# Kernel optimization log

Hardware: AMD Instinct MI355X
Metric: run time of the kernel (lower is better)

The kernel has to match this reference:

```python
import jax, jax.numpy as jnp
import numpy as np

D_MODEL = 1024; EXPAND = 2; D_INNER = 2048; D_STATE = 64; NGROUPS = 1
HEADDIM = 64; NHEADS = 32; D_CONV = 7; CHUNK = 256
CONV_DIM = D_INNER + 2 * NGROUPS * D_STATE            # 2176
D_IN_PROJ = 2 * D_INNER + 2 * NGROUPS * D_STATE + NHEADS  # 4256


def setup_inputs() -> dict:
    key = jax.random.key(0)
    ks = jax.random.split(key, 8)
    B, L = 2, 4096
    u = jax.random.normal(ks[0], (B, L, D_MODEL), jnp.float32)
    in_proj_w = jax.random.normal(ks[1], (D_IN_PROJ, D_MODEL), jnp.float32) * (1.0 / np.sqrt(D_MODEL))
    kscale = 1.0 / np.sqrt(D_CONV)
    conv_w = jax.random.uniform(ks[2], (CONV_DIM, 1, D_CONV), jnp.float32, -kscale, kscale)
    conv_b = jax.random.uniform(ks[3], (CONV_DIM,), jnp.float32, -kscale, kscale)
    # dt_bias init exactly as in the torch module
    dt = jnp.exp(jax.random.uniform(ks[4], (NHEADS,), jnp.float32) * (np.log(0.1) - np.log(0.001)) + np.log(0.001))
    dt = jnp.clip(dt, 1e-4)
    dt_bias = dt + jnp.log(-jnp.expm1(-dt))
    A_log = jnp.zeros((NHEADS,), jnp.float32)  # A = 1 -> A_log = 0, as in torch init
    norm_w = jnp.ones((D_INNER,), jnp.float32)
    out_proj_w = jax.random.normal(ks[5], (D_MODEL, D_INNER), jnp.float32) * (1.0 / np.sqrt(D_INNER))
    return {"u": u, "in_proj_w": in_proj_w, "conv_w": conv_w, "conv_b": conv_b,
            "dt_bias": dt_bias, "A_log": A_log, "norm_w": norm_w, "out_proj_w": out_proj_w}


def _segsum(x):
    # x: (..., T) -> (..., T, T) lower-triangular cumulative segment sums
    T = x.shape[-1]
    cs = jnp.cumsum(x, axis=-1)
    ss = cs[..., :, None] - cs[..., None, :]
    mask = jnp.tril(jnp.ones((T, T), bool))
    return jnp.where(mask, ss, -jnp.inf)


def _ssd(X, A, Bm, Cm, chunk):
    # Causal chunked SSD scan (Mamba2 'ssd_minimal_discrete').
    # X: (b,l,h,p) already multiplied by dt; A: (b,l,h) = A_h*dt; Bm/Cm: (b,l,h,n)
    b, l, h, p = X.shape
    n = Bm.shape[-1]
    c = l // chunk
    Xc = X.reshape(b, c, chunk, h, p)
    Ac = jnp.transpose(A.reshape(b, c, chunk, h), (0, 3, 1, 2))  # (b,h,c,l)
    Bc = Bm.reshape(b, c, chunk, h, n)
    Cc = Cm.reshape(b, c, chunk, h, n)
    A_cum = jnp.cumsum(Ac, axis=-1)
    Ldec = jnp.exp(_segsum(Ac))                                   # (b,h,c,l,s)
    G = jnp.einsum('bclhn,bcshn->bhcls', Cc, Bc)
    Y_diag = jnp.einsum('bhcls,bcshp->bclhp', G * Ldec, Xc)
    decay_states = jnp.exp(A_cum[..., -1:] - A_cum)               # (b,h,c,l)
    states = jnp.einsum('bclhn,bhcl,bclhp->bchpn', Bc, decay_states, Xc)
    A_last = jnp.pad(A_cum[..., -1], ((0, 0), (0, 0), (1, 0)))    # (b,h,c+1)
    decay_chunk = jnp.exp(_segsum(A_last))                        # (b,h,c+1,c+1)
    states = jnp.concatenate([jnp.zeros_like(states[:, :1]), states], axis=1)
    prev = jnp.einsum('bhzc,bchpn->bzhpn', decay_chunk, states)[:, :-1]
    Y_off = jnp.einsum('bclhn,bchpn,bhcl->bclhp', Cc, prev, jnp.exp(A_cum))
    return (Y_diag + Y_off).reshape(b, l, h, p)


def reference(u, in_proj_w, conv_w, conv_b, dt_bias, A_log, norm_w, out_proj_w):
    b, l, _ = u.shape
    zxbcdt = u @ in_proj_w.T                                      # (b,l,4256)
    z = zxbcdt[..., :D_INNER]
    xBC = zxbcdt[..., D_INNER:D_INNER + CONV_DIM]
    dt = jax.nn.softplus(zxbcdt[..., D_INNER + CONV_DIM:] + dt_bias)  # (b,l,h)
    # depthwise causal-padded conv1d ('same' padding, kernel 7)
    xBC = jax.lax.conv_general_dilated(
        jnp.transpose(xBC, (0, 2, 1)), conv_w, (1,), [(D_CONV // 2, D_CONV // 2)],
        dimension_numbers=('NCH', 'OIH', 'NCH'), feature_group_count=CONV_DIM)
    xBC = jax.nn.silu(jnp.transpose(xBC + conv_b[None, :, None], (0, 2, 1)))
    x = xBC[..., :D_INNER].reshape(b, l, NHEADS, HEADDIM)
    Bm = xBC[..., D_INNER:D_INNER + NGROUPS * D_STATE].reshape(b, l, NGROUPS, D_STATE)
    Cm = xBC[..., D_INNER + NGROUPS * D_STATE:].reshape(b, l, NGROUPS, D_STATE)
    Bm = jnp.repeat(Bm, NHEADS // NGROUPS, axis=2)                # broadcast groups to heads
    Cm = jnp.repeat(Cm, NHEADS // NGROUPS, axis=2)
    A = -jnp.exp(A_log)                                           # (h,)
    a = dt * A                                                    # (b,l,h)
    Xdt = x * dt[..., None]
    y_f = _ssd(Xdt, a, Bm, Cm, CHUNK)
    flip = lambda t: t[:, ::-1]
    y_b = flip(_ssd(flip(Xdt), flip(a), flip(Bm), flip(Cm), CHUNK))
    # bidirectional combine: fwd + bwd minus double-counted t==s diagonal term
    diag = jnp.einsum('blhn,blhn->blh', Cm, Bm)[..., None] * Xdt
    y = (y_f + y_b - diag).reshape(b, l, D_INNER)
    # RMSNormGated with norm_before_gate=True: rmsnorm(y) * w * silu(z)
    rstd = jax.lax.rsqrt(jnp.mean(y * y, axis=-1, keepdims=True) + 1e-5)
    y = (y * rstd) * norm_w * jax.nn.silu(z)
    return y @ out_proj_w.T
```

## Files before the change

### kernel.cpp

```cpp
#include <hip/hip_runtime.h>
#include <math.h>

#define BB 2
#define LL 4096
#define DM 1024
#define DI 2048
#define NH 32
#define HD 64
#define NSTATE 64
#define CONVD 2176
#define RAWC 2208
#define NC 16
#define CK 256
#define CTL 128

typedef __attribute__((ext_vector_type(8))) short bf16x8;
typedef __attribute__((ext_vector_type(8))) _Float16 f16x8;
typedef __attribute__((ext_vector_type(4))) float f32x4;

#define WAITVM(N) asm volatile("s_waitcnt vmcnt(" #N ")" ::: "memory")
#define WAITLGKM0 asm volatile("s_waitcnt lgkmcnt(0)" ::: "memory")

__device__ __forceinline__ float sigmoidf_(float x) { return 1.f / (1.f + expf(-x)); }
__device__ __forceinline__ float softplusf_(float x) { return (x > 20.f) ? x : log1pf(expf(x)); }

__device__ __forceinline__ unsigned short f2bf(float v) {
    unsigned u = __float_as_uint(v);
    unsigned r = (u + 0x7FFFu + ((u >> 16) & 1u)) >> 16;
    return (unsigned short)r;
}
__device__ __forceinline__ float bf2f(unsigned short h) {
    return __uint_as_float(((unsigned)h) << 16);
}

__device__ __forceinline__ int swz(int row, int col) {
    return row * 64 + ((((col >> 3) ^ (row & 7)) << 3) | (col & 7));
}

typedef const __attribute__((address_space(1))) void gvoid_t;
typedef __attribute__((address_space(3))) void lvoid_t;
__device__ __forceinline__ void gload_lds16(const void* g, void* l) {
    __builtin_amdgcn_global_load_lds((gvoid_t*)g, (lvoid_t*)l, 16, 0, 0);
}


__global__ __launch_bounds__(256) void pack_a16(const float* __restrict__ X,
                                                _Float16* __restrict__ Y, int n) {
    int idx = blockIdx.x * 256 + threadIdx.x;
    if (idx < n) Y[idx] = (_Float16)X[idx];
}

__global__ __launch_bounds__(256) void pack_w16(const float* __restrict__ W,
                                                _Float16* __restrict__ Y,
                                                int N, int Npad, int K) {
    int idx = blockIdx.x * 256 + threadIdx.x;
    if (idx >= Npad * K) return;
    int n = idx / K;
    Y[idx] = (n < N) ? (_Float16)W[idx] : (_Float16)0.f;
}

__global__ __launch_bounds__(256) void gemm_f16(const _Float16* __restrict__ A,
                                                const _Float16* __restrict__ B,
                                                float* __restrict__ C,
                                                int M, int N, int K) {
    __shared__ _Float16 As[128 * 32];
    __shared__ _Float16 Bs[128 * 32];
    int tid = threadIdx.x;
    int lane = tid & 63;
    int w = tid >> 6;
    int wr = w >> 1, wc = w & 1;
    int n0 = blockIdx.x * 128, m0 = blockIdx.y * 128;
    f32x4 acc[4][4] = {};

    for (int k0 = 0; k0 < K; k0 += 32) {
        #pragma unroll
        for (int p = 0; p < 2; ++p) {
            int s = p * 256 + tid;
            int row = s >> 2;
            int sub = (s & 3) ^ ((row >> 1) & 3);
            gload_lds16(A + (size_t)(m0 + row) * K + k0 + sub * 8, &As[s * 8]);
            gload_lds16(B + (size_t)(n0 + row) * K + k0 + sub * 8, &Bs[s * 8]);
        }
        __syncthreads();
        f16x8 af[4], bfv[4];
        #pragma unroll
        for (int i = 0; i < 4; ++i) {
            int rowA = wr * 64 + i * 16 + (lane & 15);
            int slotA = (lane >> 4) ^ ((rowA >> 1) & 3);
            af[i] = *(const f16x8*)&As[rowA * 32 + slotA * 8];
            int rowB = wc * 64 + i * 16 + (lane & 15);
            int slotB = (lane >> 4) ^ ((rowB >> 1) & 3);
            bfv[i] = *(const f16x8*)&Bs[rowB * 32 + slotB * 8];
        }
        #pragma unroll
        for (int i = 0; i < 4; ++i)
            #pragma unroll
            for (int j = 0; j < 4; ++j)
                acc[i][j] = __builtin_amdgcn_mfma_f32_16x16x32_f16(af[i], bfv[j], acc[i][j], 0, 0, 0);
        __syncthreads();
    }

    #pragma unroll
    for (int i = 0; i < 4; ++i) {
        int mbase = m0 + wr * 64 + i * 16 + (lane >> 4) * 4;
        #pragma unroll
        for (int j = 0; j < 4; ++j) {
            int n = n0 + wc * 64 + j * 16 + (lane & 15);
            if (n < N) {
                #pragma unroll
                for (int r = 0; r < 4; ++r)
                    C[(size_t)(mbase + r) * N + n] = acc[i][j][r];
            }
        }
    }
}


__global__ __launch_bounds__(256) void conv_silu(const float* __restrict__ raw,
                                                 const float* __restrict__ cw,
                                                 const float* __restrict__ cb,
                                                 float* __restrict__ xbc) {
    int ch = blockIdx.x * 256 + threadIdx.x;
    if (ch >= CONVD) return;
    int l0 = blockIdx.y * CTL;
    int b = blockIdx.z;
    float wt[7];
    #pragma unroll
    for (int j = 0; j < 7; ++j) wt[j] = cw[ch * 7 + j];
    float bias = cb[ch];
    const float* rbase = raw + (size_t)b * LL * RAWC + ch;
    float win[7];
    #pragma unroll
    for (int j = 0; j < 6; ++j) {
        int lj = l0 - 3 + j;
        win[j] = (lj >= 0 && lj < LL) ? rbase[(size_t)lj * RAWC] : 0.f;
    }
    size_t obase = ((size_t)b * LL + l0) * CONVD + ch;
    for (int i = 0; i < CTL; ++i) {
        int lj = l0 + i + 3;
        win[6] = (lj < LL) ? rbase[(size_t)lj * RAWC] : 0.f;
        float acc = bias;
        #pragma unroll
        for (int j = 0; j < 7; ++j) acc += wt[j] * win[j];
        xbc[obase + (size_t)i * CONVD] = acc * sigmoidf_(acc);
        #pragma unroll
        for (int j = 0; j < 6; ++j) win[j] = win[j + 1];
    }
}

__global__ __launch_bounds__(256) void dt_kernel(const float* __restrict__ raw,
                                                 const float* __restrict__ dt_bias,
                                                 float* __restrict__ dtb) {
    int idx = blockIdx.x * 256 + threadIdx.x;
    if (idx >= BB * LL * NH) return;
    int h = idx & 31;
    int row = idx >> 5;
    float x = raw[(size_t)row * RAWC + CONVD + h] + dt_bias[h];
    dtb[idx] = softplusf_(x);
}


__device__ __forceinline__ float block_scan256(float v, float* sc, int tid) {
    sc[tid] = v;
    __syncthreads();
    for (int off = 1; off < 256; off <<= 1) {
        float t = 0.f;
        if (tid >= off) t = sc[tid - off];
        __syncthreads();
        sc[tid] += t;
        __syncthreads();
    }
    return sc[tid];
}

__global__ __launch_bounds__(256) void g_mfma(const float* __restrict__ xbc,
                                              unsigned short* __restrict__ Gth,
                                              unsigned short* __restrict__ Gtl,
                                              int dir) {
    int lt = blockIdx.x, st = blockIdx.y, bc = blockIdx.z;
    if (st > lt) return;
    int b = bc / NC, c = bc % NC;
    int tid = threadIdx.x, lane = tid & 63, w = tid >> 6;
    __shared__ short Ch[4096], Cl[4096], Bh[4096], Bl[4096];
    #pragma unroll
    for (int i = 0; i < 16; ++i) {
        int e = tid + i * 256;
        int r = e >> 6, q = e & 63;
        int il = c * CK + lt * 64 + r;
        int tl = dir ? (LL - 1 - il) : il;
        float cv = xbc[((size_t)b * LL + tl) * CONVD + DI + NSTATE + q];
        unsigned short chh = f2bf(cv);
        Ch[swz(r, q)] = chh;
        Cl[swz(r, q)] = f2bf(cv - bf2f(chh));
        int is = c * CK + st * 64 + r;
        int ts = dir ? (LL - 1 - is) : is;
        float bv = xbc[((size_t)b * LL + ts) * CONVD + DI + q];
        unsigned short bhh = f2bf(bv);
        Bh[swz(r, q)] = bhh;
        Bl[swz(r, q)] = f2bf(bv - bf2f(bhh));
    }
    __syncthreads();
    f32x4 acc[4] = {};
    #pragma unroll
    for (int kk = 0; kk < 64; kk += 32) {
        int arow = w * 16 + (lane & 15);
        int aslot = ((kk >> 3) + (lane >> 4)) ^ (arow & 7);
        bf16x8 ah = *(const bf16x8*)&Ch[arow * 64 + aslot * 8];
        bf16x8 al = *(const bf16x8*)&Cl[arow * 64 + aslot * 8];
        #pragma unroll
        for (int j = 0; j < 4; ++j) {
            int brow = j * 16 + (lane & 15);
            int bslot = ((kk >> 3) + (lane >> 4)) ^ (brow & 7);
            bf16x8 bh = *(const bf16x8*)&Bh[brow * 64 + bslot * 8];
            bf16x8 bl = *(const bf16x8*)&Bl[brow * 64 + bslot * 8];
            acc[j] = __builtin_amdgcn_mfma_f32_16x16x32_bf16(ah, bh, acc[j], 0, 0, 0);
            acc[j] = __builtin_amdgcn_mfma_f32_16x16x32_bf16(ah, bl, acc[j], 0, 0, 0);
            acc[j] = __builtin_amdgcn_mfma_f32_16x16x32_bf16(al, bh, acc[j], 0, 0, 0);
        }
    }
    size_t tbase = ((size_t)bc * 10 + (size_t)(lt * (lt + 1) / 2 + st)) * 4096;
    #pragma unroll
    for (int j = 0; j < 4; ++j)
        #pragma unroll
        for (int rr = 0; rr < 4; ++rr) {
            int row = w * 16 + (lane >> 4) * 4 + rr;
            int col = j * 16 + (lane & 15);
            float g = acc[j][rr];
            if (lt == st && (col + dir > row)) g = 0.f;
            unsigned short hi = f2bf(g);
            int si = swz(row, col);
            Gth[tbase + si] = hi;
            Gtl[tbase + si] = f2bf(g - bf2f(hi));
        }
}

__global__ __launch_bounds__(256) void s1_mfma(const float* __restrict__ xbc,
                                               const float* __restrict__ dtb,
                                               const float* __restrict__ A_log,
                                               float* __restrict__ states,
                                               float* __restrict__ csum, int dir) {
    int h = blockIdx.x, c = blockIdx.y, b = blockIdx.z;
    int tid = threadIdx.x, lane = tid & 63, w = tid >> 6;
    __shared__ float sc[256];
    {
        int gi = c * CK + tid;
        int t = dir ? (LL - 1 - gi) : gi;
        float A = -expf(A_log[h]);
        float dtv = dtb[((size_t)b * LL + t) * NH + h];
        float acum = block_scan256(dtv * A, sc, tid);
        float cs = sc[255];
        if (tid == 0) csum[(b * NC + c) * NH + h] = cs;
        float wgt = expf(cs - acum) * dtv;
        __syncthreads();
        sc[tid] = wgt;
        __syncthreads();
    }
    __shared__ short XTh[4096], XTl[4096], BTh[4096], BTl[4096];
    f32x4 acc[4] = {};
    #pragma unroll
    for (int st = 0; st < 4; ++st) {
        #pragma unroll
        for (int i = 0; i < 16; ++i) {
            int e = tid + i * 256;
            int r = e >> 6, q = e & 63;
            int gs = c * CK + st * 64 + r;
            int ts = dir ? (LL - 1 - gs) : gs;
            size_t rowb = ((size_t)b * LL + ts) * CONVD;
            float xv = xbc[rowb + h * 64 + q] * sc[st * 64 + r];
            unsigned short xh = f2bf(xv);
            XTh[swz(q, r)] = xh;
            XTl[swz(q, r)] = f2bf(xv - bf2f(xh));
            float bv = xbc[rowb + DI + q];
            unsigned short bh_ = f2bf(bv);
            BTh[swz(q, r)] = bh_;
            BTl[swz(q, r)] = f2bf(bv - bf2f(bh_));
        }
        __syncthreads();
        #pragma unroll
        for (int kk = 0; kk < 64; kk += 32) {
            int arow = w * 16 + (lane & 15);
            int aslot = ((kk >> 3) + (lane >> 4)) ^ (arow & 7);
            bf16x8 ah = *(const bf16x8*)&XTh[arow * 64 + aslot * 8];
            bf16x8 al = *(const bf16x8*)&XTl[arow * 64 + aslot * 8];
            #pragma unroll
            for (int j = 0; j < 4; ++j) {
                int brow = j * 16 + (lane & 15);
                int bslot = ((kk >> 3) + (lane >> 4)) ^ (brow & 7);
                bf16x8 bh = *(const bf16x8*)&BTh[brow * 64 + bslot * 8];
                bf16x8 bl = *(const bf16x8*)&BTl[brow * 64 + bslot * 8];
                acc[j] = __builtin_amdgcn_mfma_f32_16x16x32_bf16(ah, bh, acc[j], 0, 0, 0);
                acc[j] = __builtin_amdgcn_mfma_f32_16x16x32_bf16(ah, bl, acc[j], 0, 0, 0);
                acc[j] = __builtin_amdgcn_mfma_f32_16x16x32_bf16(al, bh, acc[j], 0, 0, 0);
            }
        }
        __syncthreads();
    }
    size_t base = (((size_t)(b * NC + c) * NH + h)) * 4096;
    #pragma unroll
    for (int j = 0; j < 4; ++j)
        #pragma unroll
        for (int rr = 0; rr < 4; ++rr) {
            int p = w * 16 + (lane >> 4) * 4 + rr;
            int n = j * 16 + (lane & 15);
            states[base + p * 64 + n] = acc[j][rr];
        }
}

__global__ __launch_bounds__(256) void s2_scan(float* __restrict__ states,
                                               const float* __restrict__ csum) {
    int h = blockIdx.x, b = blockIdx.y, eo = blockIdx.z;
    int e = eo * 256 + threadIdx.x;
    float run = 0.f;
    for (int z = 0; z < NC; ++z) {
        size_t base = (((size_t)(b * NC + z) * NH + h)) * (64 * 64);
        float s = states[base + e];
        states[base + e] = run;
        float g = expf(csum[(b * NC + z) * NH + h]);
        run = run * g + s;
    }
}

__global__ __launch_bounds__(256) void s3_pipe(const float* __restrict__ xbc,
                                               const float* __restrict__ dtb,
                                               const float* __restrict__ A_log,
                                               const unsigned short* __restrict__ Gth,
                                               const unsigned short* __restrict__ Gtl,
                                               const float* __restrict__ prev,
                                               float* __restrict__ y, int dir, int beta) {
    int h = blockIdx.x, bc = blockIdx.y;
    int b = bc / NC, c = bc % NC;
    int tid = threadIdx.x, lane = tid & 63, w = tid >> 6;

    __shared__ short Xh[4][4096], Xl[4][4096];
    __shared__ short Gh[3][4096], Gl[3][4096];
    __shared__ float sEl[256], sEin[256];

    {
        int gi = c * CK + tid;
        int t = dir ? (LL - 1 - gi) : gi;
        float A = -expf(A_log[h]);
        float dtv = dtb[((size_t)b * LL + t) * NH + h];
        float acum = block_scan256(dtv * A, sEl, tid);
        sEl[tid] = expf(acum);
        sEin[tid] = expf(-acum) * dtv;
    }
    __syncthreads();

    constexpr int tri_[10] = {0, 1, 3, 6, 2, 4, 7, 5, 8, 9};
    auto issueA = [&](int i) {
        size_t tb = ((size_t)bc * 10 + tri_[i]) * 4096;
        int slot = i % 3;
        int o = w * 1024 + lane * 8;
        gload_lds16(Gth + tb + o,       &Gh[slot][o]);
        gload_lds16(Gth + tb + o + 512, &Gh[slot][o + 512]);
        gload_lds16(Gtl + tb + o,       &Gl[slot][o]);
        gload_lds16(Gtl + tb + o + 512, &Gl[slot][o + 512]);
    };
    issueA(0); issueA(1); issueA(2);

    #pragma unroll
    for (int st = 0; st < 4; ++st)
        #pragma unroll
        for (int i2 = 0; i2 < 16; ++i2) {
            int e = tid + i2 * 256;
            int r = e >> 6, q = e & 63;
            int gs = c * CK + st * 64 + r;
            int ts = dir ? (LL - 1 - gs) : gs;
            float xv = xbc[((size_t)b * LL + ts) * CONVD + h * 64 + q] * sEin[st * 64 + r];
            unsigned short xh = f2bf(xv);
            Xh[st][swz(q, r)] = xh;
            Xl[st][swz(q, r)] = f2bf(xv - bf2f(xh));
        }

    __builtin_amdgcn_sched_barrier(0);
    WAITLGKM0;
    __builtin_amdgcn_s_barrier();

    f32x4 acc[4][4] = {};
    constexpr int ph_lq[10] = {0, 1, 2, 3, 1, 2, 3, 2, 3, 3};
    constexpr int ph_st[10] = {0, 0, 0, 0, 1, 1, 1, 2, 2, 3};
    #pragma unroll
    for (int i = 0; i < 10; ++i) {
        const int lq = ph_lq[i], st = ph_st[i], slot = i % 3;
        if (i < 8)       { WAITVM(8); }
        else if (i == 8) { WAITVM(4); }
        else             { WAITVM(0); }
        __builtin_amdgcn_sched_barrier(0);
        int arow = w * 16 + (lane & 15);
        int s0 = (lane >> 4) ^ (arow & 7);
        int s1 = (4 + (lane >> 4)) ^ (arow & 7);
        bf16x8 ah0 = *(const bf16x8*)&Gh[slot][arow * 64 + s0 * 8];
        bf16x8 al0 = *(const bf16x8*)&Gl[slot][arow * 64 + s0 * 8];
        bf16x8 ah1 = *(const bf16x8*)&Gh[slot][arow * 64 + s1 * 8];
        bf16x8 al1 = *(const bf16x8*)&Gl[slot][arow * 64 + s1 * 8];
        bf16x8 bh0[4], bl0[4], bh1[4], bl1[4];
        #pragma unroll
        for (int j = 0; j < 4; ++j) {
            int brow = j * 16 + (lane & 15);
            int t0 = (lane >> 4) ^ (brow & 7);
            int t1 = (4 + (lane >> 4)) ^ (brow & 7);
            bh0[j] = *(const bf16x8*)&Xh[st][brow * 64 + t0 * 8];
            bl0[j] = *(const bf16x8*)&Xl[st][brow * 64 + t0 * 8];
            bh1[j] = *(const bf16x8*)&Xh[st][brow * 64 + t1 * 8];
            bl1[j] = *(const bf16x8*)&Xl[st][brow * 64 + t1 * 8];
        }
        WAITLGKM0;
        __builtin_amdgcn_sched_barrier(0);
        if (i + 3 < 10) issueA(i + 3);
        __builtin_amdgcn_sched_barrier(0);
        #pragma unroll
        for (int j = 0; j < 4; ++j) {
            acc[lq][j] = __builtin_amdgcn_mfma_f32_16x16x32_bf16(ah0, bh0[j], acc[lq][j], 0, 0, 0);
            acc[lq][j] = __builtin_amdgcn_mfma_f32_16x16x32_bf16(ah0, bl0[j], acc[lq][j], 0, 0, 0);
            acc[lq][j] = __builtin_amdgcn_mfma_f32_16x16x32_bf16(al0, bh0[j], acc[lq][j], 0, 0, 0);
            acc[lq][j] = __builtin_amdgcn_mfma_f32_16x16x32_bf16(ah1, bh1[j], acc[lq][j], 0, 0, 0);
            acc[lq][j] = __builtin_amdgcn_mfma_f32_16x16x32_bf16(ah1, bl1[j], acc[lq][j], 0, 0, 0);
            acc[lq][j] = __builtin_amdgcn_mfma_f32_16x16x32_bf16(al1, bh1[j], acc[lq][j], 0, 0, 0);
        }
    }

    __syncthreads();
    {
        size_t pbase = ((size_t)bc * NH + h) * 4096;
        #pragma unroll
        for (int i2 = 0; i2 < 16; ++i2) {
            int e = tid + i2 * 256;
            int r = e >> 6, q = e & 63;
            float pv = prev[pbase + r * 64 + q];
            unsigned short ph = f2bf(pv);
            Xh[0][swz(r, q)] = ph;
            Xl[0][swz(r, q)] = f2bf(pv - bf2f(ph));
            int il = c * CK + r;
            int tl = dir ? (LL - 1 - il) : il;
            float cv = xbc[((size_t)b * LL + tl) * CONVD + DI + NSTATE + q];
            unsigned short chh = f2bf(cv);
            Gh[0][swz(r, q)] = chh;
            Gl[0][swz(r, q)] = f2bf(cv - bf2f(chh));
        }
        __syncthreads();
        #pragma unroll
        for (int lq = 0; lq < 4; ++lq) {
            if (lq < 3) {
                #pragma unroll
                for (int i2 = 0; i2 < 16; ++i2) {
                    int e = tid + i2 * 256;
                    int r = e >> 6, q = e & 63;
                    int il = c * CK + (lq + 1) * 64 + r;
                    int tl = dir ? (LL - 1 - il) : il;
                    float cv = xbc[((size_t)b * LL + tl) * CONVD + DI + NSTATE + q];
                    unsigned short chh = f2bf(cv);
                    Gh[(lq + 1) & 1][swz(r, q)] = chh;
                    Gl[(lq + 1) & 1][swz(r, q)] = f2bf(cv - bf2f(chh));
                }
            }
            int arow = w * 16 + (lane & 15);
            int s0 = (lane >> 4) ^ (arow & 7);
            int s1 = (4 + (lane >> 4)) ^ (arow & 7);
            bf16x8 ah0 = *(const bf16x8*)&Gh[lq & 1][arow * 64 + s0 * 8];
            bf16x8 al0 = *(const bf16x8*)&Gl[lq & 1][arow * 64 + s0 * 8];
            bf16x8 ah1 = *(const bf16x8*)&Gh[lq & 1][arow * 64 + s1 * 8];
            bf16x8 al1 = *(const bf16x8*)&Gl[lq & 1][arow * 64 + s1 * 8];
            #pragma unroll
            for (int j = 0; j < 4; ++j) {
                int brow = j * 16 + (lane & 15);
                int t0 = (lane >> 4) ^ (brow & 7);
                int t1 = (4 + (lane >> 4)) ^ (brow & 7);
                bf16x8 bh0 = *(const bf16x8*)&Xh[0][brow * 64 + t0 * 8];
                bf16x8 bl0 = *(const bf16x8*)&Xl[0][brow * 64 + t0 * 8];
                bf16x8 bh1 = *(const bf16x8*)&Xh[0][brow * 64 + t1 * 8];
                bf16x8 bl1 = *(const bf16x8*)&Xl[0][brow * 64 + t1 * 8];
                acc[lq][j] = __builtin_amdgcn_mfma_f32_16x16x32_bf16(ah0, bh0, acc[lq][j], 0, 0, 0);
                acc[lq][j] = __builtin_amdgcn_mfma_f32_16x16x32_bf16(ah0, bl0, acc[lq][j], 0, 0, 0);
                acc[lq][j] = __builtin_amdgcn_mfma_f32_16x16x32_bf16(al0, bh0, acc[lq][j], 0, 0, 0);
                acc[lq][j] = __builtin_amdgcn_mfma_f32_16x16x32_bf16(ah1, bh1, acc[lq][j], 0, 0, 0);
                acc[lq][j] = __builtin_amdgcn_mfma_f32_16x16x32_bf16(ah1, bl1, acc[lq][j], 0, 0, 0);
                acc[lq][j] = __builtin_amdgcn_mfma_f32_16x16x32_bf16(al1, bh1, acc[lq][j], 0, 0, 0);
            }
            __syncthreads();
        }
    }

    #pragma unroll
    for (int lq = 0; lq < 4; ++lq)
        #pragma unroll
        for (int j = 0; j < 4; ++j)
            #pragma unroll
            for (int rr = 0; rr < 4; ++rr) {
                int ll = lq * 64 + w * 16 + (lane >> 4) * 4 + rr;
                int il = c * CK + ll;
                int tl = dir ? (LL - 1 - il) : il;
                size_t yb = ((size_t)b * LL + tl) * DI + h * 64 + j * 16 + (lane & 15);
                float v = sEl[ll] * acc[lq][j][rr];
                if (beta) y[yb] += v;
                else      y[yb]  = v;
            }
}

__global__ __launch_bounds__(256) void norm_gate16(const float* __restrict__ zbuf,
                                                   const float* __restrict__ norm_w,
                                                   const float* __restrict__ y,
                                                   _Float16* __restrict__ y16) {
    int row = blockIdx.x;
    int tid = threadIdx.x;
    float ss = 0.f;
    size_t yb = (size_t)row * DI;
    for (int i = tid; i < DI; i += 256) {
        float v = y[yb + i];
        ss += v * v;
    }
    #pragma unroll
    for (int off = 32; off > 0; off >>= 1) ss += __shfl_down(ss, off, 64);
    __shared__ float red[4];
    if ((tid & 63) == 0) red[tid >> 6] = ss;
    __syncthreads();
    float tot = red[0] + red[1] + red[2] + red[3];
    float rstd = rsqrtf(tot / DI + 1e-5f);
    for (int i = tid; i < DI; i += 256) {
        float z = zbuf[yb + i];
        float g = z * sigmoidf_(z);
        y16[yb + i] = (_Float16)(y[yb + i] * rstd * norm_w[i] * g);
    }
}

extern "C" void kernel_launch(void* const* d_in, const int* in_sizes, int n_in,
                              void* d_out, int out_size, void* d_ws, size_t ws_size,
                              hipStream_t stream) {
    const float* u          = (const float*)d_in[0];
    const float* in_proj_w  = (const float*)d_in[1];
    const float* conv_w     = (const float*)d_in[2];
    const float* conv_b     = (const float*)d_in[3];
    const float* dt_bias    = (const float*)d_in[4];
    const float* A_log      = (const float*)d_in[5];
    const float* norm_w     = (const float*)d_in[6];
    const float* out_proj_w = (const float*)d_in[7];
    float* out = (float*)d_out;

    float* ws  = (float*)d_ws;
    float* z   = ws;
    float* raw = z + (size_t)BB * LL * DI;
    float* xbc = raw + (size_t)BB * LL * RAWC;
    float* y   = raw;

    _Float16* u16    = (_Float16*)d_out;
    _Float16* w16z   = (_Float16*)xbc;
    _Float16* w16raw = w16z + (size_t)2048 * 1024;
    _Float16* w16out = (_Float16*)xbc;
    _Float16* y16    = w16out + (size_t)1024 * 2048;

    float* states        = (float*)d_out;
    unsigned short* Gth  = (unsigned short*)(states + 4194304);
    unsigned short* Gtl  = Gth + 2621440;
    float* dtb           = (float*)(Gtl + 2621440);
    float* csum          = dtb + 262144;
    float* prev          = states;

    dim3 blk(256);
    int M = BB * LL;

    pack_a16<<<(M * DM + 255) / 256, blk, 0, stream>>>(u, u16, M * DM);
    pack_w16<<<(2048 * DM + 255) / 256, blk, 0, stream>>>(in_proj_w, w16z, 2048, 2048, DM);
    pack_w16<<<(2304 * DM + 255) / 256, blk, 0, stream>>>(in_proj_w + (size_t)DI * DM, w16raw, RAWC, 2304, DM);
    gemm_f16<<<dim3(2048 / 128, M / 128), blk, 0, stream>>>(u16, w16z, z, M, 2048, DM);
    gemm_f16<<<dim3(2304 / 128, M / 128), blk, 0, stream>>>(u16, w16raw, raw, M, RAWC, DM);
    conv_silu<<<dim3((CONVD + 255) / 256, LL / CTL, BB), blk, 0, stream>>>(raw, conv_w, conv_b, xbc);
    dt_kernel<<<(BB * LL * NH + 255) / 256, blk, 0, stream>>>(raw, dt_bias, dtb);
    for (int dir = 0; dir < 2; ++dir) {
        g_mfma<<<dim3(4, 4, BB * NC), blk, 0, stream>>>(xbc, Gth, Gtl, dir);
        s1_mfma<<<dim3(NH, NC, BB), blk, 0, stream>>>(xbc, dtb, A_log, states, csum, dir);
        s2_scan<<<dim3(NH, BB, 16), blk, 0, stream>>>(states, csum);
        s3_pipe<<<dim3(NH, BB * NC), blk, 0, stream>>>(xbc, dtb, A_log, Gth, Gtl, prev, y, dir, dir);
    }
    norm_gate16<<<M, blk, 0, stream>>>(z, norm_w, y, y16);
    pack_a16<<<(DM * DI + 255) / 256, blk, 0, stream>>>(out_proj_w, w16out, DM * DI);
    gemm_f16<<<dim3(1024 / 128, M / 128), blk, 0, stream>>>(y16, w16out, out, M, DM, DI);
}
```

Measured before the change: 688.0 us.

## Double-buffer X and G tiles in s3_pipe to fit two blocks per CU

s3_pipe previously staged all four X sub-tiles (hi and lo bf16) plus a triple-buffered G pipeline in LDS, about 114 KB per block. That allowed only one block per CU. The change keeps two X slots and two G slots, refilling X sub-tiles inside the MFMA loop with extra barriers at phase boundaries, and sets launch_bounds(256,2). The goal is to fit two resident blocks per CU so one block's global-load latency can hide behind the other's MFMAs. The cost is a shallower prefetch, more block-wide barriers, and X conversion work serialized into the compute loop.

```diff
diff --git a/kernel.cpp b/kernel.cpp
--- a/kernel.cpp
+++ b/kernel.cpp
@@ -320,19 +320,19 @@
     }
 }
 
-__global__ __launch_bounds__(256) void s3_pipe(const float* __restrict__ xbc,
-                                               const float* __restrict__ dtb,
-                                               const float* __restrict__ A_log,
-                                               const unsigned short* __restrict__ Gth,
-                                               const unsigned short* __restrict__ Gtl,
-                                               const float* __restrict__ prev,
-                                               float* __restrict__ y, int dir, int beta) {
+__global__ __launch_bounds__(256, 2) void s3_pipe(const float* __restrict__ xbc,
+                                                  const float* __restrict__ dtb,
+                                                  const float* __restrict__ A_log,
+                                                  const unsigned short* __restrict__ Gth,
+                                                  const unsigned short* __restrict__ Gtl,
+                                                  const float* __restrict__ prev,
+                                                  float* __restrict__ y, int dir, int beta) {
     int h = blockIdx.x, bc = blockIdx.y;
     int b = bc / NC, c = bc % NC;
     int tid = threadIdx.x, lane = tid & 63, w = tid >> 6;
 
-    __shared__ short Xh[4][4096], Xl[4][4096];
-    __shared__ short Gh[3][4096], Gl[3][4096];
+    __shared__ short Xh[2][4096], Xl[2][4096];
+    __shared__ short Gh[2][4096], Gl[2][4096];
     __shared__ float sEl[256], sEin[256];
 
     {
@@ -349,17 +349,15 @@
     constexpr int tri_[10] = {0, 1, 3, 6, 2, 4, 7, 5, 8, 9};
     auto issueA = [&](int i) {
         size_t tb = ((size_t)bc * 10 + tri_[i]) * 4096;
-        int slot = i % 3;
+        int slot = i & 1;
         int o = w * 1024 + lane * 8;
         gload_lds16(Gth + tb + o,       &Gh[slot][o]);
         gload_lds16(Gth + tb + o + 512, &Gh[slot][o + 512]);
         gload_lds16(Gtl + tb + o,       &Gl[slot][o]);
         gload_lds16(Gtl + tb + o + 512, &Gl[slot][o + 512]);
     };
-    issueA(0); issueA(1); issueA(2);
-
-    #pragma unroll
-    for (int st = 0; st < 4; ++st)
+    auto stageX = [&](int st) {
+        int slot = st & 1;
         #pragma unroll
         for (int i2 = 0; i2 < 16; ++i2) {
             int e = tid + i2 * 256;
@@ -368,9 +366,13 @@
             int ts = dir ? (LL - 1 - gs) : gs;
             float xv = xbc[((size_t)b * LL + ts) * CONVD + h * 64 + q] * sEin[st * 64 + r];
             unsigned short xh = f2bf(xv);
-            Xh[st][swz(q, r)] = xh;
-            Xl[st][swz(q, r)] = f2bf(xv - bf2f(xh));
-        }
+            Xh[slot][swz(q, r)] = xh;
+            Xl[slot][swz(q, r)] = f2bf(xv - bf2f(xh));
+        }
+    };
+
+    issueA(0); issueA(1);
+    stageX(0);
 
     __builtin_amdgcn_sched_barrier(0);
     WAITLGKM0;
@@ -381,10 +383,14 @@
     constexpr int ph_st[10] = {0, 0, 0, 0, 1, 1, 1, 2, 2, 3};
     #pragma unroll
     for (int i = 0; i < 10; ++i) {
-        const int lq = ph_lq[i], st = ph_st[i], slot = i % 3;
-        if (i < 8)       { WAITVM(8); }
-        else if (i == 8) { WAITVM(4); }
-        else             { WAITVM(0); }
+        const int lq = ph_lq[i], st = ph_st[i], slot = i & 1, xslot = st & 1;
+        if (i == 4 || i == 7 || i == 9) {
+            __builtin_amdgcn_sched_barrier(0);
+            WAITLGKM0;
+            __builtin_amdgcn_s_barrier();
+        }
+        if (i < 9) { WAITVM(4); }
+        else       { WAITVM(0); }
         __builtin_amdgcn_sched_barrier(0);
         int arow = w * 16 + (lane & 15);
         int s0 = (lane >> 4) ^ (arow & 7);
@@ -399,15 +405,18 @@
             int brow = j * 16 + (lane & 15);
             int t0 = (lane >> 4) ^ (brow & 7);
             int t1 = (4 + (lane >> 4)) ^ (brow & 7);
-            bh0[j] = *(const bf16x8*)&Xh[st][brow * 64 + t0 * 8];
-            bl0[j] = *(const bf16x8*)&Xl[st][brow * 64 + t0 * 8];
-            bh1[j] = *(const bf16x8*)&Xh[st][brow * 64 + t1 * 8];
-            bl1[j] = *(const bf16x8*)&Xl[st][brow * 64 + t1 * 8];
+            bh0[j] = *(const bf16x8*)&Xh[xslot][brow * 64 + t0 * 8];
+            bl0[j] = *(const bf16x8*)&Xl[xslot][brow * 64 + t0 * 8];
+            bh1[j] = *(const bf16x8*)&Xh[xslot][brow * 64 + t1 * 8];
+            bl1[j] = *(const bf16x8*)&Xl[xslot][brow * 64 + t1 * 8];
         }
         WAITLGKM0;
         __builtin_amdgcn_sched_barrier(0);
-        if (i + 3 < 10) issueA(i + 3);
+        if (i + 2 < 10) issueA(i + 2);
         __builtin_amdgcn_sched_barrier(0);
+        if (i == 0)      stageX(1);
+        else if (i == 4) stageX(2);
+        else if (i == 7) stageX(3);
         #pragma unroll
         for (int j = 0; j < 4; ++j) {
             acc[lq][j] = __builtin_amdgcn_mfma_f32_16x16x32_bf16(ah0, bh0[j], acc[lq][j], 0, 0, 0);
```

Measured after the change: 764.7 us. 1.11x slower.

## Load G and C operands directly into registers instead of staging through LDS

Applied to the files above, without the earlier changes.

The s3 kernel stops staging the precomputed G tiles through a triple-buffered async global-to-LDS pipeline. Each wave now loads its MFMA A-operand fragments straight from global memory into registers, and g_mfma writes G unswizzled to match. The C-matrix operand for the inter-chunk term is likewise read from global and split into hi/lo bf16 in registers, replacing the LDS double-buffer and its per-iteration barriers. This cuts LDS use (raising occupancy) and removes syncs, but exposes global-load latency with no explicit prefetch and issues strided, uncoalesced float reads for C.

```diff
diff --git a/kernel.cpp b/kernel.cpp
--- a/kernel.cpp
+++ b/kernel.cpp
@@ -17,9 +17,6 @@
 typedef __attribute__((ext_vector_type(8))) short bf16x8;
 typedef __attribute__((ext_vector_type(8))) _Float16 f16x8;
 typedef __attribute__((ext_vector_type(4))) float f32x4;
-
-#define WAITVM(N) asm volatile("s_waitcnt vmcnt(" #N ")" ::: "memory")
-#define WAITLGKM0 asm volatile("s_waitcnt lgkmcnt(0)" ::: "memory")
 
 __device__ __forceinline__ float sigmoidf_(float x) { return 1.f / (1.f + expf(-x)); }
 __device__ __forceinline__ float softplusf_(float x) { return (x > 20.f) ? x : log1pf(expf(x)); }
@@ -228,7 +225,7 @@
             float g = acc[j][rr];
             if (lt == st && (col + dir > row)) g = 0.f;
             unsigned short hi = f2bf(g);
-            int si = swz(row, col);
+            int si = row * 64 + col;
             Gth[tbase + si] = hi;
             Gtl[tbase + si] = f2bf(g - bf2f(hi));
         }
@@ -320,19 +317,18 @@
     }
 }
 
-__global__ __launch_bounds__(256) void s3_pipe(const float* __restrict__ xbc,
-                                               const float* __restrict__ dtb,
-                                               const float* __restrict__ A_log,
-                                               const unsigned short* __restrict__ Gth,
-                                               const unsigned short* __restrict__ Gtl,
-                                               const float* __restrict__ prev,
-                                               float* __restrict__ y, int dir, int beta) {
+__global__ __launch_bounds__(256) void s3_reg(const float* __restrict__ xbc,
+                                              const float* __restrict__ dtb,
+                                              const float* __restrict__ A_log,
+                                              const unsigned short* __restrict__ Gth,
+                                              const unsigned short* __restrict__ Gtl,
+                                              const float* __restrict__ prev,
+                                              float* __restrict__ y, int dir, int beta) {
     int h = blockIdx.x, bc = blockIdx.y;
     int b = bc / NC, c = bc % NC;
     int tid = threadIdx.x, lane = tid & 63, w = tid >> 6;
 
     __shared__ short Xh[4][4096], Xl[4][4096];
-    __shared__ short Gh[3][4096], Gl[3][4096];
     __shared__ float sEl[256], sEin[256];
 
     {
@@ -345,18 +341,6 @@
         sEin[tid] = expf(-acum) * dtv;
     }
     __syncthreads();
-
-    constexpr int tri_[10] = {0, 1, 3, 6, 2, 4, 7, 5, 8, 9};
-    auto issueA = [&](int i) {
-        size_t tb = ((size_t)bc * 10 + tri_[i]) * 4096;
-        int slot = i % 3;
-        int o = w * 1024 + lane * 8;
-        gload_lds16(Gth + tb + o,       &Gh[slot][o]);
-        gload_lds16(Gth + tb + o + 512, &Gh[slot][o + 512]);
-        gload_lds16(Gtl + tb + o,       &Gl[slot][o]);
-        gload_lds16(Gtl + tb + o + 512, &Gl[slot][o + 512]);
-    };
-    issueA(0); issueA(1); issueA(2);
 
     #pragma unroll
     for (int st = 0; st < 4; ++st)
@@ -371,51 +355,37 @@
             Xh[st][swz(q, r)] = xh;
             Xl[st][swz(q, r)] = f2bf(xv - bf2f(xh));
         }
-
-    __builtin_amdgcn_sched_barrier(0);
-    WAITLGKM0;
-    __builtin_amdgcn_s_barrier();
+    __syncthreads();
 
     f32x4 acc[4][4] = {};
+    const int arow = w * 16 + (lane & 15);
+    const int kofs = (lane >> 4) * 8;
     constexpr int ph_lq[10] = {0, 1, 2, 3, 1, 2, 3, 2, 3, 3};
     constexpr int ph_st[10] = {0, 0, 0, 0, 1, 1, 1, 2, 2, 3};
     #pragma unroll
     for (int i = 0; i < 10; ++i) {
-        const int lq = ph_lq[i], st = ph_st[i], slot = i % 3;
-        if (i < 8)       { WAITVM(8); }
-        else if (i == 8) { WAITVM(4); }
-        else             { WAITVM(0); }
-        __builtin_amdgcn_sched_barrier(0);
-        int arow = w * 16 + (lane & 15);
-        int s0 = (lane >> 4) ^ (arow & 7);
-        int s1 = (4 + (lane >> 4)) ^ (arow & 7);
-        bf16x8 ah0 = *(const bf16x8*)&Gh[slot][arow * 64 + s0 * 8];
-        bf16x8 al0 = *(const bf16x8*)&Gl[slot][arow * 64 + s0 * 8];
-        bf16x8 ah1 = *(const bf16x8*)&Gh[slot][arow * 64 + s1 * 8];
-        bf16x8 al1 = *(const bf16x8*)&Gl[slot][arow * 64 + s1 * 8];
-        bf16x8 bh0[4], bl0[4], bh1[4], bl1[4];
+        const int lq = ph_lq[i], st = ph_st[i];
+        size_t tb = ((size_t)bc * 10 + (size_t)(lq * (lq + 1) / 2 + st)) * 4096
+                  + (size_t)arow * 64 + kofs;
+        bf16x8 ah0 = *(const bf16x8*)(Gth + tb);
+        bf16x8 ah1 = *(const bf16x8*)(Gth + tb + 32);
+        bf16x8 al0 = *(const bf16x8*)(Gtl + tb);
+        bf16x8 al1 = *(const bf16x8*)(Gtl + tb + 32);
         #pragma unroll
         for (int j = 0; j < 4; ++j) {
             int brow = j * 16 + (lane & 15);
             int t0 = (lane >> 4) ^ (brow & 7);
             int t1 = (4 + (lane >> 4)) ^ (brow & 7);
-            bh0[j] = *(const bf16x8*)&Xh[st][brow * 64 + t0 * 8];
-            bl0[j] = *(const bf16x8*)&Xl[st][brow * 64 + t0 * 8];
-            bh1[j] = *(const bf16x8*)&Xh[st][brow * 64 + t1 * 8];
-            bl1[j] = *(const bf16x8*)&Xl[st][brow * 64 + t1 * 8];
-        }
-        WAITLGKM0;
-        __builtin_amdgcn_sched_barrier(0);
-        if (i + 3 < 10) issueA(i + 3);
-        __builtin_amdgcn_sched_barrier(0);
-        #pragma unroll
-        for (int j = 0; j < 4; ++j) {
-            acc[lq][j] = __builtin_amdgcn_mfma_f32_16x16x32_bf16(ah0, bh0[j], acc[lq][j], 0, 0, 0);
-            acc[lq][j] = __builtin_amdgcn_mfma_f32_16x16x32_bf16(ah0, bl0[j], acc[lq][j], 0, 0, 0);
-            acc[lq][j] = __builtin_amdgcn_mfma_f32_16x16x32_bf16(al0, bh0[j], acc[lq][j], 0, 0, 0);
-            acc[lq][j] = __builtin_amdgcn_mfma_f32_16x16x32_bf16(ah1, bh1[j], acc[lq][j], 0, 0, 0);
-            acc[lq][j] = __builtin_amdgcn_mfma_f32_16x16x32_bf16(ah1, bl1[j], acc[lq][j], 0, 0, 0);
-            acc[lq][j] = __builtin_amdgcn_mfma_f32_16x16x32_bf16(al1, bh1[j], acc[lq][j], 0, 0, 0);
+            bf16x8 bh0 = *(const bf16x8*)&Xh[st][brow * 64 + t0 * 8];
+            bf16x8 bl0 = *(const bf16x8*)&Xl[st][brow * 64 + t0 * 8];
+            bf16x8 bh1 = *(const bf16x8*)&Xh[st][brow * 64 + t1 * 8];
+            bf16x8 bl1 = *(const bf16x8*)&Xl[st][brow * 64 + t1 * 8];
+            acc[lq][j] = __builtin_amdgcn_mfma_f32_16x16x32_bf16(ah0, bh0, acc[lq][j], 0, 0, 0);
+            acc[lq][j] = __builtin_amdgcn_mfma_f32_16x16x32_bf16(ah0, bl0, acc[lq][j], 0, 0, 0);
+            acc[lq][j] = __builtin_amdgcn_mfma_f32_16x16x32_bf16(al0, bh0, acc[lq][j], 0, 0, 0);
+            acc[lq][j] = __builtin_amdgcn_mfma_f32_16x16x32_bf16(ah1, bh1, acc[lq][j], 0, 0, 0);
+            acc[lq][j] = __builtin_amdgcn_mfma_f32_16x16x32_bf16(ah1, bl1, acc[lq][j], 0, 0, 0);
+            acc[lq][j] = __builtin_amdgcn_mfma_f32_16x16x32_bf16(al1, bh1, acc[lq][j], 0, 0, 0);
         }
     }
 
@@ -430,53 +400,39 @@
             unsigned short ph = f2bf(pv);
             Xh[0][swz(r, q)] = ph;
             Xl[0][swz(r, q)] = f2bf(pv - bf2f(ph));
-            int il = c * CK + r;
-            int tl = dir ? (LL - 1 - il) : il;
-            float cv = xbc[((size_t)b * LL + tl) * CONVD + DI + NSTATE + q];
-            unsigned short chh = f2bf(cv);
-            Gh[0][swz(r, q)] = chh;
-            Gl[0][swz(r, q)] = f2bf(cv - bf2f(chh));
-        }
-        __syncthreads();
-        #pragma unroll
-        for (int lq = 0; lq < 4; ++lq) {
-            if (lq < 3) {
-                #pragma unroll
-                for (int i2 = 0; i2 < 16; ++i2) {
-                    int e = tid + i2 * 256;
-                    int r = e >> 6, q = e & 63;
-                    int il = c * CK + (lq + 1) * 64 + r;
-                    int tl = dir ? (LL - 1 - il) : il;
-                    float cv = xbc[((size_t)b * LL + tl) * CONVD + DI + NSTATE + q];
-                    unsigned short chh = f2bf(cv);
-                    Gh[(lq + 1) & 1][swz(r, q)] = chh;
-                    Gl[(lq + 1) & 1][swz(r, q)] = f2bf(cv - bf2f(chh));
-                }
-            }
-            int arow = w * 16 + (lane & 15);
-            int s0 = (lane >> 4) ^ (arow & 7);
-            int s1 = (4 + (lane >> 4)) ^ (arow & 7);
-            bf16x8 ah0 = *(const bf16x8*)&Gh[lq & 1][arow * 64 + s0 * 8];
-            bf16x8 al0 = *(const bf16x8*)&Gl[lq & 1][arow * 64 + s0 * 8];
-            bf16x8 ah1 = *(const bf16x8*)&Gh[lq & 1][arow * 64 + s1 * 8];
-            bf16x8 al1 = *(const bf16x8*)&Gl[lq & 1][arow * 64 + s1 * 8];
-            #pragma unroll
-            for (int j = 0; j < 4; ++j) {
-                int brow = j * 16 + (lane & 15);
-                int t0 = (lane >> 4) ^ (brow & 7);
-                int t1 = (4 + (lane >> 4)) ^ (brow & 7);
-                bf16x8 bh0 = *(const bf16x8*)&Xh[0][brow * 64 + t0 * 8];
-                bf16x8 bl0 = *(const bf16x8*)&Xl[0][brow * 64 + t0 * 8];
-                bf16x8 bh1 = *(const bf16x8*)&Xh[0][brow * 64 + t1 * 8];
-                bf16x8 bl1 = *(const bf16x8*)&Xl[0][brow * 64 + t1 * 8];
-                acc[lq][j] = __builtin_amdgcn_mfma_f32_16x16x32_bf16(ah0, bh0, acc[lq][j], 0, 0, 0);
-                acc[lq][j] = __builtin_amdgcn_mfma_f32_16x16x32_bf16(ah0, bl0, acc[lq][j], 0, 0, 0);
-                acc[lq][j] = __builtin_amdgcn_mfma_f32_16x16x32_bf16(al0, bh0, acc[lq][j], 0, 0, 0);
-                acc[lq][j] = __builtin_amdgcn_mfma_f32_16x16x32_bf16(ah1, bh1, acc[lq][j], 0, 0, 0);
-                acc[lq][j] = __builtin_amdgcn_mfma_f32_16x16x32_bf16(ah1, bl1, acc[lq][j], 0, 0, 0);
-                acc[lq][j] = __builtin_amdgcn_mfma_f32_16x16x32_bf16(al1, bh1, acc[lq][j], 0, 0, 0);
-            }
-            __syncthreads();
+        }
+    }
+    __syncthreads();
+    #pragma unroll
+    for (int lq = 0; lq < 4; ++lq) {
+        int il = c * CK + lq * 64 + arow;
+        int tl = dir ? (LL - 1 - il) : il;
+        const float* cp = xbc + ((size_t)b * LL + tl) * CONVD + DI + NSTATE;
+        bf16x8 ah0, al0, ah1, al1;
+        #pragma unroll
+        for (int e = 0; e < 8; ++e) {
+            float c0 = cp[kofs + e];
+            float c1 = cp[32 + kofs + e];
+            unsigned short hh = f2bf(c0);
+            ah0[e] = (short)hh; al0[e] = (short)f2bf(c0 - bf2f(hh));
+            hh = f2bf(c1);
+            ah1[e] = (short)hh; al1[e] = (short)f2bf(c1 - bf2f(hh));
+        }
+        #pragma unroll
+        for (int j = 0; j < 4; ++j) {
+            int brow = j * 16 + (lane & 15);
+            int t0 = (lane >> 4) ^ (brow & 7);
+            int t1 = (4 + (lane >> 4)) ^ (brow & 7);
+            bf16x8 bh0 = *(const bf16x8*)&Xh[0][brow * 64 + t0 * 8];
+            bf16x8 bl0 = *(const bf16x8*)&Xl[0][brow * 64 + t0 * 8];
+            bf16x8 bh1 = *(const bf16x8*)&Xh[0][brow * 64 + t1 * 8];
+            bf16x8 bl1 = *(const bf16x8*)&Xl[0][brow * 64 + t1 * 8];
+            acc[lq][j] = __builtin_amdgcn_mfma_f32_16x16x32_bf16(ah0, bh0, acc[lq][j], 0, 0, 0);
+            acc[lq][j] = __builtin_amdgcn_mfma_f32_16x16x32_bf16(ah0, bl0, acc[lq][j], 0, 0, 0);
+            acc[lq][j] = __builtin_amdgcn_mfma_f32_16x16x32_bf16(al0, bh0, acc[lq][j], 0, 0, 0);
+            acc[lq][j] = __builtin_amdgcn_mfma_f32_16x16x32_bf16(ah1, bh1, acc[lq][j], 0, 0, 0);
+            acc[lq][j] = __builtin_amdgcn_mfma_f32_16x16x32_bf16(ah1, bl1, acc[lq][j], 0, 0, 0);
+            acc[lq][j] = __builtin_amdgcn_mfma_f32_16x16x32_bf16(al1, bh1, acc[lq][j], 0, 0, 0);
         }
     }
 
@@ -568,7 +524,7 @@
         g_mfma<<<dim3(4, 4, BB * NC), blk, 0, stream>>>(xbc, Gth, Gtl, dir);
         s1_mfma<<<dim3(NH, NC, BB), blk, 0, stream>>>(xbc, dtb, A_log, states, csum, dir);
         s2_scan<<<dim3(NH, BB, 16), blk, 0, stream>>>(states, csum);
-        s3_pipe<<<dim3(NH, BB * NC), blk, 0, stream>>>(xbc, dtb, A_log, Gth, Gtl, prev, y, dir, dir);
+        s3_reg<<<dim3(NH, BB * NC), blk, 0, stream>>>(xbc, dtb, A_log, Gth, Gtl, prev, y, dir, dir);
     }
     norm_gate16<<<M, blk, 0, stream>>>(z, norm_w, y, y16);
     pack_a16<<<(DM * DI + 255) / 256, blk, 0, stream>>>(out_proj_w, w16out, DM * DI);
```

Result: faster. 629.6 us (-8.5%).
